# Kernel tuning notes

Hardware: AMD Instinct MI355X
Metric: run time of the kernel (lower is better)

## Reference

```python
import jax, jax.numpy as jnp
import numpy as np

D_IN = 2048; D_OUT = 2048; DL = 512; NUM_HEAD = 16; CTX = 2048
HEAD_DIM = D_OUT // NUM_HEAD  # 128


def setup_inputs() -> dict:
    key = jax.random.key(0)
    ks = jax.random.split(key, 20)
    s = 0.02
    def lin(k, din, dout):
        k1, k2 = jax.random.split(k)
        return (jax.random.normal(k1, (din, dout), jnp.float32) * s,
                jax.random.normal(k2, (dout,), jnp.float32) * s)
    w_kv, b_kv = lin(ks[0], D_IN, DL)
    w_ku, b_ku = lin(ks[1], DL, D_OUT // 2)
    w_kr, b_kr = lin(ks[2], D_IN, D_OUT // 2)
    w_vu, b_vu = lin(ks[3], DL, D_OUT)
    w_q,  b_q  = lin(ks[4], D_IN, DL)
    w_qu, b_qu = lin(ks[5], DL, D_OUT // 2)
    w_qr, b_qr = lin(ks[6], DL, D_OUT // 2)
    w_o,  b_o  = lin(ks[7], D_OUT, D_OUT)
    x = jax.random.normal(ks[8], (2, 2048, D_IN), jnp.float32)
    return dict(x=x, w_kv=w_kv, b_kv=b_kv, w_ku=w_ku, b_ku=b_ku, w_kr=w_kr, b_kr=b_kr,
                w_vu=w_vu, b_vu=b_vu, w_q=w_q, b_q=b_q, w_qu=w_qu, b_qu=b_qu,
                w_qr=w_qr, b_qr=b_qr, w_o=w_o, b_o=b_o)


def reference(x, w_kv, b_kv, w_ku, b_ku, w_kr, b_kr, w_vu, b_vu,
              w_q, b_q, w_qu, b_qu, w_qr, b_qr, w_o, b_o):
    b, s, _ = x.shape
    # latent KV compression
    ckv = x @ w_kv + b_kv                                   # (b, s, dl)
    # NOTE: source Rope.forward is a no-op (returns input), replicated faithfully.
    key = jnp.concatenate([ckv @ w_ku + b_ku, x @ w_kr + b_kr], axis=-1)   # (b, s, d_out)
    q_lat = x @ w_q + b_q                                   # (b, s, dl)
    query = jnp.concatenate([q_lat @ w_qu + b_qu, q_lat @ w_qr + b_qr], axis=-1)
    value = ckv @ w_vu + b_vu                               # (b, s, d_out)
    # split heads -> (b, h, s, hd)
    def heads(t):
        return t.reshape(b, s, NUM_HEAD, HEAD_DIM).transpose(0, 2, 1, 3)
    q, k, v = heads(query), heads(key), heads(value)
    scores = jnp.einsum('bhqd,bhkd->bhqk', q, k)
    causal = jnp.tril(jnp.ones((s, s), dtype=bool))
    scores = jnp.where(causal, scores, -jnp.inf)
    at = jax.nn.softmax(scores / jnp.sqrt(jnp.float32(HEAD_DIM)), axis=-1)
    # dropout rate 0 -> identity
    out = jnp.einsum('bhqk,bhkd->bhqd', at, v).transpose(0, 2, 1, 3).reshape(b, s, D_OUT)
    return out @ w_o + b_o
```

## Files before the change

kernel.cpp:

```cpp
#include <hip/hip_runtime.h>
#include <hip/hip_bf16.h>

typedef __hip_bfloat16 bf16;
typedef __bf16 bf16_t;
typedef __bf16 bf16x8 __attribute__((ext_vector_type(8)));
typedef __bf16 bf16x4v __attribute__((ext_vector_type(4)));
typedef float f32x4 __attribute__((ext_vector_type(4)));

#define D_IN 2048
#define D_OUT 2048
#define DL 512
#define NUM_HEAD 16
#define SEQ 2048
#define HEAD_DIM 128
#define BATCH 2
#define NTOK (BATCH * SEQ)

__device__ __forceinline__ void stf(float* p, float v) { *p = v; }
__device__ __forceinline__ void stf(bf16_t* p, float v) { *p = (bf16_t)v; }

__device__ __forceinline__ void async_cp16(const bf16_t* g, bf16_t* l) {
    __builtin_amdgcn_global_load_lds(
        (const __attribute__((address_space(1))) void*)g,
        (__attribute__((address_space(3))) void*)l, 16, 0, 0);
}

#define CVTB 8192
#define NTOPS 8

struct TOp { const float* W; bf16_t* Wt; int K, N, nx, nblk; };
struct TOps { TOp op[NTOPS]; };

__global__ __launch_bounds__(256) void prep_kernel(
    const float* __restrict__ x, bf16_t* __restrict__ xb,
    TOps ops,
    const float* __restrict__ b_kv, const float* __restrict__ b_q,
    float* __restrict__ bkvq,
    const float* __restrict__ b_qu, const float* __restrict__ b_qr,
    float* __restrict__ bquqr, int trb)
{
    const int tid = threadIdx.x;
    int blk = blockIdx.x;

    if (blk < CVTB) {
        int i = (blk * 256 + tid) * 4;
        float4 v = *(const float4*)&x[i];
        bf16_t o[4] = {(bf16_t)v.x, (bf16_t)v.y, (bf16_t)v.z, (bf16_t)v.w};
        *(ulong1*)&xb[i] = *(ulong1*)o;
        return;
    }
    blk -= CVTB;
    if (blk < trb) {
        int op = 0;
        while (blk >= ops.op[op].nblk) { blk -= ops.op[op].nblk; ++op; }
        const TOp& t = ops.op[op];
        const int n0 = (blk % t.nx) * 32, k0 = (blk / t.nx) * 32;
        __shared__ float tl[32][33];
        const int c = tid & 31, r0 = tid >> 5;
#pragma unroll
        for (int rr = 0; rr < 32; rr += 8)
            tl[r0 + rr][c] = t.W[(size_t)(k0 + r0 + rr) * t.N + n0 + c];
        __syncthreads();
#pragma unroll
        for (int rr = 0; rr < 32; rr += 8)
            t.Wt[(size_t)(n0 + r0 + rr) * t.K + k0 + c] = (bf16_t)tl[c][r0 + rr];
        return;
    }
    blk -= trb;
    if (blk == 0) {
#pragma unroll
        for (int j = 0; j < 4; ++j) {
            int i = tid + j * 256;
            bkvq[i] = (i < DL) ? b_kv[i] : b_q[i - DL];
        }
    } else {
#pragma unroll
        for (int j = 0; j < 8; ++j) {
            int i = tid + j * 256;
            bquqr[i] = (i < 1024) ? b_qu[i] : b_qr[i - 1024];
        }
    }
}

struct GOp { const bf16_t* A; const bf16_t* Wt; const float* bias;
             void* C; int lda, K, col0, ldc, nx, nblk; };
template <int N> struct GOps { GOp op[N]; };

template <typename TC, int NOPS>
__global__ __launch_bounds__(256) void gemm_multi_kernel(GOps<NOPS> ops)
{
    __shared__ __align__(16) bf16_t As[2 * 128 * 32];
    __shared__ __align__(16) bf16_t Bs[2 * 128 * 32];

    int blk = blockIdx.x;
    int opi = 0;
    while (blk >= ops.op[opi].nblk) { blk -= ops.op[opi].nblk; ++opi; }
    const GOp& g = ops.op[opi];

    const int tid  = threadIdx.x;
    const int wave = tid >> 6, lane = tid & 63;
    const int quad = lane >> 4, l16 = lane & 15;
    const int wm = wave & 1, wn = wave >> 1;
    const int m0 = (blk / g.nx) * 128;
    const int n0 = (blk % g.nx) * 128;

    const int r0 = tid >> 2, c0 = (tid & 3) * 8;
    const bf16_t* Ap0 = g.A  + (size_t)(m0 + r0)      * g.lda + c0;
    const bf16_t* Ap1 = g.A  + (size_t)(m0 + r0 + 64) * g.lda + c0;
    const bf16_t* Bp0 = g.Wt + (size_t)(n0 + r0)      * g.K   + c0;
    const bf16_t* Bp1 = g.Wt + (size_t)(n0 + r0 + 64) * g.K   + c0;

    f32x4 acc[4][4];
#pragma unroll
    for (int i = 0; i < 4; ++i)
#pragma unroll
        for (int j = 0; j < 4; ++j) acc[i][j] = (f32x4){0.f, 0.f, 0.f, 0.f};

    for (int k0 = 0; k0 < g.K; k0 += 64) {
        __syncthreads();
#pragma unroll
        for (int p = 0; p < 2; ++p) {
            async_cp16(Ap0 + k0 + p * 32, As + p * 4096 + tid * 8);
            async_cp16(Ap1 + k0 + p * 32, As + p * 4096 + 2048 + tid * 8);
            async_cp16(Bp0 + k0 + p * 32, Bs + p * 4096 + tid * 8);
            async_cp16(Bp1 + k0 + p * 32, Bs + p * 4096 + 2048 + tid * 8);
        }
        __syncthreads();

#pragma unroll
        for (int p = 0; p < 2; ++p) {
            bf16x8 af[4], bfr[4];
#pragma unroll
            for (int t = 0; t < 4; ++t) {
                af[t]  = *(const bf16x8*)&As[p * 4096 + (wm * 64 + t * 16 + l16) * 32 + quad * 8];
                bfr[t] = *(const bf16x8*)&Bs[p * 4096 + (wn * 64 + t * 16 + l16) * 32 + quad * 8];
            }
#pragma unroll
            for (int mt = 0; mt < 4; ++mt)
#pragma unroll
                for (int nt = 0; nt < 4; ++nt)
                    acc[mt][nt] = __builtin_amdgcn_mfma_f32_16x16x32_bf16(
                        af[mt], bfr[nt], acc[mt][nt], 0, 0, 0);
        }
    }

    TC* C = (TC*)g.C;
    const int mrow = m0 + wm * 64 + quad * 4;
#pragma unroll
    for (int mt = 0; mt < 4; ++mt)
#pragma unroll
        for (int nt = 0; nt < 4; ++nt) {
            int col = n0 + wn * 64 + nt * 16 + l16;
            float bv = g.bias[col];
#pragma unroll
            for (int r = 0; r < 4; ++r)
                stf(&C[(size_t)(mrow + mt * 16 + r) * g.ldc + g.col0 + col],
                    acc[mt][nt][r] + bv);
        }
}

#define KS_LD 136
#define VT_LD 72
#define P_LD  72
#define NQT   (SEQ / 64)

__global__ __launch_bounds__(256) void attn_mfma_kernel(
    bf16_t* __restrict__ Qg, const bf16_t* __restrict__ Kg,
    const bf16_t* __restrict__ Vg)
{
    __shared__ __align__(16) bf16_t Ks[64 * KS_LD];
    __shared__ __align__(16) bf16_t Vt[128 * VT_LD];
    __shared__ __align__(16) bf16_t Pls[4 * 16 * P_LD];

    const int tid  = threadIdx.x;
    const int wave = tid >> 6;
    const int lane = tid & 63;
    const int quad = lane >> 4;
    const int l16  = lane & 15;

    const int grp = blockIdx.x & 31;
    const int h   = grp & 15;
    const int b   = grp >> 4;
    const int p   = blockIdx.x >> 5;
    const int qtA = p, qtB = NQT - 1 - p;
    const int ntiles = qtB + 1;

    const int base = b * SEQ;
    const int hd0  = h * HEAD_DIM;
    const float scale = 0.08838834764831845f;
    bf16_t* Pw = Pls + wave * 16 * P_LD;

    bf16x8 qfA[4], qfB[4];
    {
        const bf16_t* qa = Qg + (size_t)(base + qtA * 64 + wave * 16 + l16) * D_OUT + hd0;
        const bf16_t* qb = Qg + (size_t)(base + qtB * 64 + wave * 16 + l16) * D_OUT + hd0;
#pragma unroll
        for (int kb = 0; kb < 4; ++kb) {
            qfA[kb] = *(const bf16x8*)(qa + kb * 32 + quad * 8);
            qfB[kb] = *(const bf16x8*)(qb + kb * 32 + quad * 8);
        }
    }

    f32x4 oA[8], oB[8];
#pragma unroll
    for (int ob = 0; ob < 8; ++ob) {
        oA[ob] = (f32x4){0.f, 0.f, 0.f, 0.f};
        oB[ob] = (f32x4){0.f, 0.f, 0.f, 0.f};
    }
    float mA = -INFINITY, mB = -INFINITY, lA = 0.f, lB = 0.f;

    const int rk = tid >> 4, ck = (tid & 15) * 8;
    const int kg = (tid & 15) * 4, dg = tid >> 4;

    bf16x8 kpre[4], vpre[4];
    auto issue = [&](int k0) {
#pragma unroll
        for (int jj = 0; jj < 4; ++jj)
            kpre[jj] = *(const bf16x8*)&Kg[(size_t)(base + k0 + rk + 16 * jj) * D_OUT + hd0 + ck];
#pragma unroll
        for (int kk = 0; kk < 4; ++kk)
            vpre[kk] = *(const bf16x8*)&Vg[(size_t)(base + k0 + kg + kk) * D_OUT + hd0 + dg * 8];
    };
    issue(0);

    auto process = [&](const bf16x8* qf, f32x4* o, float& m_i, float& l_i,
                       int qt, int k0) {
        f32x4 s[4];
#pragma unroll
        for (int nb = 0; nb < 4; ++nb) s[nb] = (f32x4){0.f, 0.f, 0.f, 0.f};
#pragma unroll
        for (int kb = 0; kb < 4; ++kb)
#pragma unroll
            for (int nb = 0; nb < 4; ++nb) {
                bf16x8 kfrag = *(const bf16x8*)&Ks[(nb * 16 + l16) * KS_LD + kb * 32 + quad * 8];
                s[nb] = __builtin_amdgcn_mfma_f32_16x16x32_bf16(kfrag, qf[kb], s[nb], 0, 0, 0);
            }

        const int qabs = qt * 64 + wave * 16 + l16;
        if (k0 + 63 <= qt * 64 + wave * 16) {
#pragma unroll
            for (int nb = 0; nb < 4; ++nb)
#pragma unroll
                for (int r = 0; r < 4; ++r) s[nb][r] *= scale;
        } else {
#pragma unroll
            for (int nb = 0; nb < 4; ++nb) {
                int key = k0 + nb * 16 + quad * 4;
#pragma unroll
                for (int r = 0; r < 4; ++r)
                    s[nb][r] = (key + r <= qabs) ? s[nb][r] * scale : -INFINITY;
            }
        }

        float rmax = -INFINITY;
#pragma unroll
        for (int nb = 0; nb < 4; ++nb)
#pragma unroll
            for (int r = 0; r < 4; ++r) rmax = fmaxf(rmax, s[nb][r]);
        rmax = fmaxf(rmax, __shfl_xor(rmax, 16, 64));
        rmax = fmaxf(rmax, __shfl_xor(rmax, 32, 64));

        const float mnew = fmaxf(m_i, rmax);
        const float alpha = __expf(m_i - mnew);
        m_i = mnew;

        float rs = 0.f;
#pragma unroll
        for (int nb = 0; nb < 4; ++nb)
#pragma unroll
            for (int r = 0; r < 4; ++r) {
                float pv = __expf(s[nb][r] - mnew);
                s[nb][r] = pv;
                rs += pv;
            }
        rs += __shfl_xor(rs, 16, 64);
        rs += __shfl_xor(rs, 32, 64);
        l_i = l_i * alpha + rs;

#pragma unroll
        for (int ob = 0; ob < 8; ++ob)
#pragma unroll
            for (int r = 0; r < 4; ++r) o[ob][r] *= alpha;

#pragma unroll
        for (int nb = 0; nb < 4; ++nb) {
            bf16x4v pk = {(bf16_t)s[nb][0], (bf16_t)s[nb][1],
                          (bf16_t)s[nb][2], (bf16_t)s[nb][3]};
            *(bf16x4v*)&Pw[l16 * P_LD + nb * 16 + quad * 4] = pk;
        }
        __builtin_amdgcn_s_waitcnt(0xc07f);
        bf16x8 pb0 = *(const bf16x8*)&Pw[l16 * P_LD + 0 + quad * 8];
        bf16x8 pb1 = *(const bf16x8*)&Pw[l16 * P_LD + 32 + quad * 8];

#pragma unroll
        for (int ob = 0; ob < 8; ++ob) {
            bf16x8 v0 = *(const bf16x8*)&Vt[(ob * 16 + l16) * VT_LD + 0 + quad * 8];
            o[ob] = __builtin_amdgcn_mfma_f32_16x16x32_bf16(v0, pb0, o[ob], 0, 0, 0);
            bf16x8 v1 = *(const bf16x8*)&Vt[(ob * 16 + l16) * VT_LD + 32 + quad * 8];
            o[ob] = __builtin_amdgcn_mfma_f32_16x16x32_bf16(v1, pb1, o[ob], 0, 0, 0);
        }
    };

    for (int t = 0; t < ntiles; ++t) {
        const int k0 = t * 64;
        __syncthreads();
#pragma unroll
        for (int jj = 0; jj < 4; ++jj)
            *(bf16x8*)&Ks[(rk + 16 * jj) * KS_LD + ck] = kpre[jj];
#pragma unroll
        for (int j = 0; j < 8; ++j) {
            bf16x4v pk = {vpre[0][j], vpre[1][j], vpre[2][j], vpre[3][j]};
            *(bf16x4v*)&Vt[(dg * 8 + j) * VT_LD + kg] = pk;
        }
        __syncthreads();
        if (t + 1 < ntiles) issue(k0 + 64);

        process(qfB, oB, mB, lB, qtB, k0);
        if (t <= qtA) process(qfA, oA, mA, lA, qtA, k0);
    }

    auto writeback = [&](f32x4* o, float l_i, int qt) {
        const int q = qt * 64 + wave * 16 + l16;
        const float inv = 1.f / l_i;
        bf16_t* orow = Qg + (size_t)(base + q) * D_OUT + hd0;
#pragma unroll
        for (int ob = 0; ob < 8; ++ob) {
            bf16x4v pk = {(bf16_t)(o[ob][0] * inv), (bf16_t)(o[ob][1] * inv),
                          (bf16_t)(o[ob][2] * inv), (bf16_t)(o[ob][3] * inv)};
            *(bf16x4v*)&orow[ob * 16 + quad * 4] = pk;
        }
    };
    writeback(oA, lA, qtA);
    writeback(oB, lB, qtB);
}

extern "C" void kernel_launch(void* const* d_in, const int* in_sizes, int n_in,
                              void* d_out, int out_size, void* d_ws, size_t ws_size,
                              hipStream_t stream)
{
    const float* x    = (const float*)d_in[0];
    const float* w_kv = (const float*)d_in[1];
    const float* b_kv = (const float*)d_in[2];
    const float* w_ku = (const float*)d_in[3];
    const float* b_ku = (const float*)d_in[4];
    const float* w_kr = (const float*)d_in[5];
    const float* b_kr = (const float*)d_in[6];
    const float* w_vu = (const float*)d_in[7];
    const float* b_vu = (const float*)d_in[8];
    const float* w_q  = (const float*)d_in[9];
    const float* b_q  = (const float*)d_in[10];
    const float* w_qu = (const float*)d_in[11];
    const float* b_qu = (const float*)d_in[12];
    const float* w_qr = (const float*)d_in[13];
    const float* b_qr = (const float*)d_in[14];
    const float* w_o  = (const float*)d_in[15];
    const float* b_o  = (const float*)d_in[16];
    float* out = (float*)d_out;

    bf16_t* ws    = (bf16_t*)d_ws;
    bf16_t* ckvq  = ws;
    bf16_t* query = ckvq  + NTOK * 1024;
    bf16_t* value = query + NTOK * D_OUT;
    bf16_t* wt_kv = value + NTOK * D_OUT;
    bf16_t* wt_q  = wt_kv + 512 * 2048;
    bf16_t* wt_ku = wt_q  + 512 * 2048;
    bf16_t* wt_kr = wt_ku + 1024 * 512;
    bf16_t* wt_vu = wt_kr + 1024 * 2048;
    bf16_t* wt_qu = wt_vu + 2048 * 512;
    bf16_t* wt_qr = wt_qu + 1024 * 512;
    bf16_t* wt_o  = wt_qr + 1024 * 512;
    float*  bkvq  = (float*)(wt_o + 2048 * 2048);
    float*  bquqr = bkvq + 1024;
    bf16_t* key   = (bf16_t*)d_out;
    bf16_t* xb    = key + NTOK * D_OUT;

    TOps tops = {{
        { w_kv, wt_kv, 2048,  512, 16,  16 * 64 },
        { w_q,  wt_q,  2048,  512, 16,  16 * 64 },
        { w_ku, wt_ku,  512, 1024, 32,  32 * 16 },
        { w_kr, wt_kr, 2048, 1024, 32,  32 * 64 },
        { w_vu, wt_vu,  512, 2048, 64,  64 * 16 },
        { w_qu, wt_qu,  512, 1024, 32,  32 * 16 },
        { w_qr, wt_qr,  512, 1024, 32,  32 * 16 },
        { w_o,  wt_o,  2048, 2048, 64,  64 * 64 },
    }};
    int trb = 0;
    for (int i = 0; i < NTOPS; ++i) trb += tops.op[i].nblk;
    prep_kernel<<<CVTB + trb + 2, 256, 0, stream>>>(
        x, xb, tops, b_kv, b_q, bkvq, b_qu, b_qr, bquqr, trb);

    GOps<1> s1 = {{
        { xb, wt_kv, bkvq, ckvq, D_IN, D_IN, 0, 1024, 8, 8 * 32 },
    }};
    gemm_multi_kernel<bf16_t, 1><<<8 * 32, 256, 0, stream>>>(s1);

    GOps<4> s2 = {{
        { xb,         wt_kr, b_kr,  key,   D_IN, 2048, 1024, D_OUT,  8, 256 },
        { ckvq + 512, wt_qu, bquqr, query, 1024,  512,    0, D_OUT, 16, 512 },
        { ckvq,       wt_vu, b_vu,  value, 1024,  512,    0, D_OUT, 16, 512 },
        { ckvq,       wt_ku, b_ku,  key,   1024,  512,    0, D_OUT,  8, 256 },
    }};
    gemm_multi_kernel<bf16_t, 4><<<1536, 256, 0, stream>>>(s2);

    attn_mfma_kernel<<<512, 256, 0, stream>>>(query, key, value);

    GOps<1> s3 = {{
        { query, wt_o, b_o, out, D_OUT, 2048, 0, D_OUT, 16, 512 },
    }};
    gemm_multi_kernel<float, 1><<<512, 256, 0, stream>>>(s3);
}
```

Measured before the change: 391.0 us.

## Split attention to one query tile per block, keep P in registers, defer rescale

Each attention block now handles one 64-row query tile instead of a pair of mirrored tiles, and the grid doubles to 1024 blocks. Tiles are handed out in a snake order to balance the causal work, and launch bounds are raised to target four blocks per CU. Keys are loaded in a permuted row order so the score MFMA output lands directly in the layout the PV MFMA needs. This removes the P round-trip through LDS and its waitcnt. The online-softmax rescale of the accumulator is skipped when every lane's new max stays within 8 of the running max, which trades some exp headroom for fewer multiplies.

```diff
diff --git a/kernel.cpp b/kernel.cpp
--- a/kernel.cpp
+++ b/kernel.cpp
@@ -161,16 +161,13 @@
 
 #define KS_LD 136
 #define VT_LD 72
-#define P_LD  72
-#define NQT   (SEQ / 64)
-
-__global__ __launch_bounds__(256) void attn_mfma_kernel(
+
+__global__ __launch_bounds__(256, 4) void attn_mfma_kernel(
     bf16_t* __restrict__ Qg, const bf16_t* __restrict__ Kg,
     const bf16_t* __restrict__ Vg)
 {
     __shared__ __align__(16) bf16_t Ks[64 * KS_LD];
     __shared__ __align__(16) bf16_t Vt[128 * VT_LD];
-    __shared__ __align__(16) bf16_t Pls[4 * 16 * P_LD];
 
     const int tid  = threadIdx.x;
     const int wave = tid >> 6;
@@ -181,50 +178,62 @@
     const int grp = blockIdx.x & 31;
     const int h   = grp & 15;
     const int b   = grp >> 4;
-    const int p   = blockIdx.x >> 5;
-    const int qtA = p, qtB = NQT - 1 - p;
-    const int ntiles = qtB + 1;
+    const int u   = blockIdx.x >> 5;
+    const int ua  = u >> 3, uc = u & 7;
+    const int qt  = 8 * ua + ((ua & 1) ? (7 - uc) : uc);
+    const int ntiles = qt + 1;
 
     const int base = b * SEQ;
     const int hd0  = h * HEAD_DIM;
     const float scale = 0.08838834764831845f;
-    bf16_t* Pw = Pls + wave * 16 * P_LD;
-
-    bf16x8 qfA[4], qfB[4];
+
+    bf16x8 qf[4];
     {
-        const bf16_t* qa = Qg + (size_t)(base + qtA * 64 + wave * 16 + l16) * D_OUT + hd0;
-        const bf16_t* qb = Qg + (size_t)(base + qtB * 64 + wave * 16 + l16) * D_OUT + hd0;
-#pragma unroll
-        for (int kb = 0; kb < 4; ++kb) {
-            qfA[kb] = *(const bf16x8*)(qa + kb * 32 + quad * 8);
-            qfB[kb] = *(const bf16x8*)(qb + kb * 32 + quad * 8);
-        }
-    }
-
-    f32x4 oA[8], oB[8];
-#pragma unroll
-    for (int ob = 0; ob < 8; ++ob) {
-        oA[ob] = (f32x4){0.f, 0.f, 0.f, 0.f};
-        oB[ob] = (f32x4){0.f, 0.f, 0.f, 0.f};
-    }
-    float mA = -INFINITY, mB = -INFINITY, lA = 0.f, lB = 0.f;
+        const bf16_t* qp = Qg + (size_t)(base + qt * 64 + wave * 16 + l16) * D_OUT + hd0;
+#pragma unroll
+        for (int kb = 0; kb < 4; ++kb)
+            qf[kb] = *(const bf16x8*)(qp + kb * 32 + quad * 8);
+    }
+
+    f32x4 o[8];
+#pragma unroll
+    for (int ob = 0; ob < 8; ++ob) o[ob] = (f32x4){0.f, 0.f, 0.f, 0.f};
+    float m_i = -INFINITY, l_i = 0.f;
 
     const int rk = tid >> 4, ck = (tid & 15) * 8;
     const int kg = (tid & 15) * 4, dg = tid >> 4;
+    const int rbase = (rk >> 2) * 8 + (rk & 3);
 
     bf16x8 kpre[4], vpre[4];
     auto issue = [&](int k0) {
-#pragma unroll
-        for (int jj = 0; jj < 4; ++jj)
-            kpre[jj] = *(const bf16x8*)&Kg[(size_t)(base + k0 + rk + 16 * jj) * D_OUT + hd0 + ck];
+        const bf16_t* kp = Kg + (size_t)(base + k0 + rbase) * D_OUT + hd0 + ck;
+        kpre[0] = *(const bf16x8*)(kp);
+        kpre[1] = *(const bf16x8*)(kp + (size_t)4  * D_OUT);
+        kpre[2] = *(const bf16x8*)(kp + (size_t)32 * D_OUT);
+        kpre[3] = *(const bf16x8*)(kp + (size_t)36 * D_OUT);
 #pragma unroll
         for (int kk = 0; kk < 4; ++kk)
             vpre[kk] = *(const bf16x8*)&Vg[(size_t)(base + k0 + kg + kk) * D_OUT + hd0 + dg * 8];
     };
     issue(0);
 
-    auto process = [&](const bf16x8* qf, f32x4* o, float& m_i, float& l_i,
-                       int qt, int k0) {
+    const int qabs = qt * 64 + wave * 16 + l16;
+    const int qwav = qt * 64 + wave * 16;
+
+    for (int t = 0; t < ntiles; ++t) {
+        const int k0 = t * 64;
+        __syncthreads();
+#pragma unroll
+        for (int jj = 0; jj < 4; ++jj)
+            *(bf16x8*)&Ks[(rk + 16 * jj) * KS_LD + ck] = kpre[jj];
+#pragma unroll
+        for (int j = 0; j < 8; ++j) {
+            bf16x4v pk = {vpre[0][j], vpre[1][j], vpre[2][j], vpre[3][j]};
+            *(bf16x4v*)&Vt[(dg * 8 + j) * VT_LD + kg] = pk;
+        }
+        __syncthreads();
+        if (t + 1 < ntiles) issue(k0 + 64);
+
         f32x4 s[4];
 #pragma unroll
         for (int nb = 0; nb < 4; ++nb) s[nb] = (f32x4){0.f, 0.f, 0.f, 0.f};
@@ -236,8 +245,7 @@
                 s[nb] = __builtin_amdgcn_mfma_f32_16x16x32_bf16(kfrag, qf[kb], s[nb], 0, 0, 0);
             }
 
-        const int qabs = qt * 64 + wave * 16 + l16;
-        if (k0 + 63 <= qt * 64 + wave * 16) {
+        if (k0 + 63 <= qwav) {
 #pragma unroll
             for (int nb = 0; nb < 4; ++nb)
 #pragma unroll
@@ -245,7 +253,7 @@
         } else {
 #pragma unroll
             for (int nb = 0; nb < 4; ++nb) {
-                int key = k0 + nb * 16 + quad * 4;
+                int key = k0 + (nb >> 1) * 32 + quad * 8 + (nb & 1) * 4;
 #pragma unroll
                 for (int r = 0; r < 4; ++r)
                     s[nb][r] = (key + r <= qabs) ? s[nb][r] * scale : -INFINITY;
@@ -260,9 +268,8 @@
         rmax = fmaxf(rmax, __shfl_xor(rmax, 16, 64));
         rmax = fmaxf(rmax, __shfl_xor(rmax, 32, 64));
 
-        const float mnew = fmaxf(m_i, rmax);
-        const float alpha = __expf(m_i - mnew);
-        m_i = mnew;
+        const bool defer = (bool)__all(rmax - m_i <= 8.f);
+        const float mnew = defer ? m_i : fmaxf(m_i, rmax);
 
         float rs = 0.f;
 #pragma unroll
@@ -275,22 +282,27 @@
             }
         rs += __shfl_xor(rs, 16, 64);
         rs += __shfl_xor(rs, 32, 64);
-        l_i = l_i * alpha + rs;
-
-#pragma unroll
-        for (int ob = 0; ob < 8; ++ob)
-#pragma unroll
-            for (int r = 0; r < 4; ++r) o[ob][r] *= alpha;
-
-#pragma unroll
-        for (int nb = 0; nb < 4; ++nb) {
-            bf16x4v pk = {(bf16_t)s[nb][0], (bf16_t)s[nb][1],
-                          (bf16_t)s[nb][2], (bf16_t)s[nb][3]};
-            *(bf16x4v*)&Pw[l16 * P_LD + nb * 16 + quad * 4] = pk;
-        }
-        __builtin_amdgcn_s_waitcnt(0xc07f);
-        bf16x8 pb0 = *(const bf16x8*)&Pw[l16 * P_LD + 0 + quad * 8];
-        bf16x8 pb1 = *(const bf16x8*)&Pw[l16 * P_LD + 32 + quad * 8];
+
+        if (!defer) {
+            const float alpha = __expf(m_i - mnew);
+            l_i = l_i * alpha + rs;
+            m_i = mnew;
+#pragma unroll
+            for (int ob = 0; ob < 8; ++ob)
+#pragma unroll
+                for (int r = 0; r < 4; ++r) o[ob][r] *= alpha;
+        } else {
+            l_i += rs;
+        }
+
+        bf16x8 pb0, pb1;
+#pragma unroll
+        for (int r = 0; r < 4; ++r) {
+            pb0[r]     = (bf16_t)s[0][r];
+            pb0[4 + r] = (bf16_t)s[1][r];
+            pb1[r]     = (bf16_t)s[2][r];
+            pb1[4 + r] = (bf16_t)s[3][r];
+        }
 
 #pragma unroll
         for (int ob = 0; ob < 8; ++ob) {
@@ -299,27 +311,9 @@
             bf16x8 v1 = *(const bf16x8*)&Vt[(ob * 16 + l16) * VT_LD + 32 + quad * 8];
             o[ob] = __builtin_amdgcn_mfma_f32_16x16x32_bf16(v1, pb1, o[ob], 0, 0, 0);
         }
-    };
-
-    for (int t = 0; t < ntiles; ++t) {
-        const int k0 = t * 64;
-        __syncthreads();
-#pragma unroll
-        for (int jj = 0; jj < 4; ++jj)
-            *(bf16x8*)&Ks[(rk + 16 * jj) * KS_LD + ck] = kpre[jj];
-#pragma unroll
-        for (int j = 0; j < 8; ++j) {
-            bf16x4v pk = {vpre[0][j], vpre[1][j], vpre[2][j], vpre[3][j]};
-            *(bf16x4v*)&Vt[(dg * 8 + j) * VT_LD + kg] = pk;
-        }
-        __syncthreads();
-        if (t + 1 < ntiles) issue(k0 + 64);
-
-        process(qfB, oB, mB, lB, qtB, k0);
-        if (t <= qtA) process(qfA, oA, mA, lA, qtA, k0);
-    }
-
-    auto writeback = [&](f32x4* o, float l_i, int qt) {
+    }
+
+    {
         const int q = qt * 64 + wave * 16 + l16;
         const float inv = 1.f / l_i;
         bf16_t* orow = Qg + (size_t)(base + q) * D_OUT + hd0;
@@ -329,9 +323,7 @@
                           (bf16_t)(o[ob][2] * inv), (bf16_t)(o[ob][3] * inv)};
             *(bf16x4v*)&orow[ob * 16 + quad * 4] = pk;
         }
-    };
-    writeback(oA, lA, qtA);
-    writeback(oB, lB, qtB);
+    }
 }
 
 extern "C" void kernel_launch(void* const* d_in, const int* in_sizes, int n_in,
@@ -402,7 +394,7 @@
     }};
     gemm_multi_kernel<bf16_t, 4><<<1536, 256, 0, stream>>>(s2);
 
-    attn_mfma_kernel<<<512, 256, 0, stream>>>(query, key, value);
+    attn_mfma_kernel<<<1024, 256, 0, stream>>>(query, key, value);
 
     GOps<1> s3 = {{
         { query, wt_o, b_o, out, D_OUT, 2048, 0, D_OUT, 16, 512 },
```

Result: slower. 399.2 us (+2.1%).
